# Kernel tuning notes

Measured on AMD Instinct MI355X. Metric: run time of the kernel, lower is better.

## Reference

```python
import jax, jax.numpy as jnp
import numpy as np

N, IN_DIM, H, K = 4096, 64, 64, 3
DT = 0.05


def graph_filter(z, S_powers, W):
    # z: [N, d_in], S_powers: [K, N, N], W: [K, d_in, d_out]
    zk = jnp.einsum('knm,md->knd', S_powers, z)   # K-hop diffused features
    return jnp.einsum('knd,kde->ne', zk, W)       # sum over taps k


def setup_inputs() -> dict:
    key = jax.random.key(0)
    ks = jax.random.split(key, 8)
    w_scale = 0.1
    return {
        'x': jax.random.normal(ks[0], (N, H), jnp.float32),
        'u': jax.random.normal(ks[1], (N, IN_DIM), jnp.float32),
        'S_powers': jax.random.normal(ks[2], (K, N, N), jnp.float32) / np.float32(np.sqrt(N)),
        'WA_hat': jax.random.normal(ks[3], (K, H, H), jnp.float32) * w_scale,
        'WB_hat': jax.random.normal(ks[4], (K, IN_DIM, H), jnp.float32) * w_scale,
        'WA_state': jax.random.normal(ks[5], (K, H, H), jnp.float32) * w_scale,
        'WB_state': jax.random.normal(ks[6], (K, IN_DIM, H), jnp.float32) * w_scale,
        'bx': jnp.zeros((1, H), jnp.float32),
        'bu': jnp.zeros((1, H), jnp.float32),
        'b': jnp.ones((1, H), jnp.float32) * 0.1,
        'n_steps': 4,
    }


def reference(x, u, S_powers, WA_hat, WB_hat, WA_state, WB_state, bx, bu, b, n_steps):
    # Input-driven terms are constant across solver steps; hoist them.
    fu = jax.nn.relu(graph_filter(u, S_powers, WB_hat) + bu)   # [N, H]
    sigma_c = jnp.tanh(graph_filter(u, S_powers, WB_state))    # [N, H]

    def step(xc, _):
        f = jax.nn.relu(graph_filter(xc, S_powers, WA_hat) + bx) + fu
        dx = -(b + f) * xc - graph_filter(xc, S_powers, WA_state) + f * sigma_c
        xn = jnp.clip(xc + DT * dx, -1.0, 1.0)
        return xn, None

    xf, _ = jax.lax.scan(step, x, None, length=n_steps)
    return xf
```

## Files before the change

kernel.cpp:

```cpp
#include <hip/hip_runtime.h>
#include <math.h>


typedef unsigned short u16;
typedef unsigned int u32;
typedef __attribute__((ext_vector_type(8))) short short8;
typedef __attribute__((ext_vector_type(4))) float f32x4;

#define NN 4096
#define HD 64
#define DT_C 0.05f

__device__ __forceinline__ u16 f2bf(float f) {
    u32 u = __float_as_uint(f);
    u += 0x7FFFu + ((u >> 16) & 1u);
    return (u16)(u >> 16);
}
__device__ __forceinline__ u32 pk2(float a, float b) {
    return (u32)f2bf(a) | ((u32)f2bf(b) << 16);
}

__global__ __launch_bounds__(256) void prep_kernel(
    const float* __restrict__ u, const float* __restrict__ x,
    const float* __restrict__ WAh, const float* __restrict__ WAs,
    const float* __restrict__ WBh, const float* __restrict__ WBs,
    u16* __restrict__ ut, u16* __restrict__ xt, u16* __restrict__ Wt)
{
    const int b = blockIdx.x;
    const int t = threadIdx.x;
    if (b < 128) {
        const float* z = (b < 64) ? u : x;
        u16* zt = (b < 64) ? ut : xt;
        const int n0 = (b & 63) * 64;
        __shared__ __align__(16) u16 tile[64][72];
        const int nl = t >> 2, c0 = (t & 3) * 16;
        const float* src = z + (size_t)(n0 + nl) * HD + c0;
        #pragma unroll
        for (int j = 0; j < 16; ++j) tile[nl][c0 + j] = f2bf(src[j]);
        __syncthreads();
        const int h = t >> 2, m0 = (t & 3) * 16;
        uint4 w0, w1;
        w0.x = (u32)tile[m0 + 0][h] | ((u32)tile[m0 + 1][h] << 16);
        w0.y = (u32)tile[m0 + 2][h] | ((u32)tile[m0 + 3][h] << 16);
        w0.z = (u32)tile[m0 + 4][h] | ((u32)tile[m0 + 5][h] << 16);
        w0.w = (u32)tile[m0 + 6][h] | ((u32)tile[m0 + 7][h] << 16);
        w1.x = (u32)tile[m0 + 8][h] | ((u32)tile[m0 + 9][h] << 16);
        w1.y = (u32)tile[m0 + 10][h] | ((u32)tile[m0 + 11][h] << 16);
        w1.z = (u32)tile[m0 + 12][h] | ((u32)tile[m0 + 13][h] << 16);
        w1.w = (u32)tile[m0 + 14][h] | ((u32)tile[m0 + 15][h] << 16);
        u16* dst = zt + (size_t)h * NN + n0 + m0;
        ((uint4*)dst)[0] = w0;
        ((uint4*)dst)[1] = w1;
    } else if (b == 128) {
        for (int f = t; f < 4 * 12288; f += 256) {
            int mat = f / 12288, rem = f % 12288;
            int e = rem / 192, kp = rem % 192;
            const float* Wm = (mat == 0) ? WAh : (mat == 1) ? WAs : (mat == 2) ? WBh : WBs;
            Wt[f] = f2bf(Wm[(size_t)kp * HD + e]);
        }
    }
}

__global__ __launch_bounds__(256) void convS_kernel(
    const float* __restrict__ S, u16* __restrict__ Sb)
{
    const size_t i = ((size_t)blockIdx.x * 256 + threadIdx.x) * 8;
    float4 f0 = *(const float4*)(S + i);
    float4 f1 = *(const float4*)(S + i + 4);
    uint4 o;
    o.x = pk2(f0.x, f0.y); o.y = pk2(f0.z, f0.w);
    o.z = pk2(f1.x, f1.y); o.w = pk2(f1.z, f1.w);
    *(uint4*)(Sb + i) = o;
}

__global__ __launch_bounds__(256) void diffuseA_kernel(
    const u16* __restrict__ Sb, const u16* __restrict__ ut,
    const u16* __restrict__ xt, float* __restrict__ Yp, int kchunk)
{
    const int t = threadIdx.x;
    const int tap = blockIdx.z;
    const int row0 = blockIdx.x * 128;
    const int kb0 = blockIdx.y * kchunk;
    const int w = t >> 6, lane = t & 63, l15 = lane & 15, quad = lane >> 4;

    const u16* A0 = Sb + (size_t)tap * NN * NN + (size_t)(row0 + w * 32 + l15) * NN + quad * 8;
    const u16* A1 = A0 + 16 * NN;

    f32x4 z4 = {0.f, 0.f, 0.f, 0.f};
    f32x4 acc[2][2][4];
    #pragma unroll
    for (int s = 0; s < 2; ++s)
        #pragma unroll
        for (int i = 0; i < 2; ++i)
            #pragma unroll
            for (int j = 0; j < 4; ++j) acc[s][i][j] = z4;

    #pragma unroll 2
    for (int kb = kb0; kb < kb0 + kchunk; kb += 32) {
        short8 a0 = *(const short8*)(A0 + kb);
        short8 a1 = *(const short8*)(A1 + kb);
        #pragma unroll
        for (int ct = 0; ct < 4; ++ct) {
            const size_t bo = (size_t)(ct * 16 + l15) * NN + kb + quad * 8;
            short8 bu = *(const short8*)(ut + bo);
            short8 bx = *(const short8*)(xt + bo);
            acc[0][0][ct] = __builtin_amdgcn_mfma_f32_16x16x32_bf16(a0, bu, acc[0][0][ct], 0, 0, 0);
            acc[0][1][ct] = __builtin_amdgcn_mfma_f32_16x16x32_bf16(a1, bu, acc[0][1][ct], 0, 0, 0);
            acc[1][0][ct] = __builtin_amdgcn_mfma_f32_16x16x32_bf16(a0, bx, acc[1][0][ct], 0, 0, 0);
            acc[1][1][ct] = __builtin_amdgcn_mfma_f32_16x16x32_bf16(a1, bx, acc[1][1][ct], 0, 0, 0);
        }
    }
    #pragma unroll
    for (int s = 0; s < 2; ++s) {
        float* yb = Yp + ((size_t)((blockIdx.y * 3 + tap) * 2 + s) * NN + row0) * HD;
        #pragma unroll
        for (int rt = 0; rt < 2; ++rt)
            #pragma unroll
            for (int ct = 0; ct < 4; ++ct)
                #pragma unroll
                for (int r = 0; r < 4; ++r)
                    yb[(size_t)(w * 32 + rt * 16 + quad * 4 + r) * HD + ct * 16 + l15] = acc[s][rt][ct][r];
    }
}

__global__ __launch_bounds__(256) void diffuseS_kernel(
    const u16* __restrict__ Sb, const u16* __restrict__ xt,
    float* __restrict__ Yp, int kchunk)
{
    const int t = threadIdx.x;
    const int tap = blockIdx.z;
    const int row0 = blockIdx.x * 128;
    const int kb0 = blockIdx.y * kchunk;
    const int w = t >> 6, lane = t & 63, l15 = lane & 15, quad = lane >> 4;

    const u16* A0 = Sb + (size_t)tap * NN * NN + (size_t)(row0 + w * 32 + l15) * NN + quad * 8;
    const u16* A1 = A0 + 16 * NN;

    f32x4 z4 = {0.f, 0.f, 0.f, 0.f};
    f32x4 acc[2][4];
    #pragma unroll
    for (int i = 0; i < 2; ++i)
        #pragma unroll
        for (int j = 0; j < 4; ++j) acc[i][j] = z4;

    #pragma unroll 2
    for (int kb = kb0; kb < kb0 + kchunk; kb += 32) {
        short8 a0 = *(const short8*)(A0 + kb);
        short8 a1 = *(const short8*)(A1 + kb);
        #pragma unroll
        for (int ct = 0; ct < 4; ++ct) {
            short8 bb = *(const short8*)(xt + (size_t)(ct * 16 + l15) * NN + kb + quad * 8);
            acc[0][ct] = __builtin_amdgcn_mfma_f32_16x16x32_bf16(a0, bb, acc[0][ct], 0, 0, 0);
            acc[1][ct] = __builtin_amdgcn_mfma_f32_16x16x32_bf16(a1, bb, acc[1][ct], 0, 0, 0);
        }
    }
    float* yb = Yp + ((size_t)(blockIdx.y * 3 + tap) * NN + row0) * HD;
    #pragma unroll
    for (int rt = 0; rt < 2; ++rt)
        #pragma unroll
        for (int ct = 0; ct < 4; ++ct)
            #pragma unroll
            for (int r = 0; r < 4; ++r)
                yb[(size_t)(w * 32 + rt * 16 + quad * 4 + r) * HD + ct * 16 + l15] = acc[rt][ct][r];
}

__global__ __launch_bounds__(256) void reduce_kernel(
    const float* __restrict__ Yp, int KS, int nsrc,
    u16* __restrict__ dst0, u16* __restrict__ dst1)
{
    const int tid = blockIdx.x * 256 + threadIdx.x;
    const int src = tid / 196608;
    const int r = tid - src * 196608;
    const int d4 = r & 15;
    const int n = (r >> 4) & 4095;
    const int tap = r >> 16;
    const float* p = Yp + ((size_t)tap * nsrc + src) * ((size_t)NN * HD)
                        + (size_t)n * HD + d4 * 4;
    const size_t kstride = (size_t)3 * nsrc * NN * HD;
    float4 s = {0.f, 0.f, 0.f, 0.f};
    for (int ks = 0; ks < KS; ++ks) {
        float4 v = *(const float4*)(p + ks * kstride);
        s.x += v.x; s.y += v.y; s.z += v.z; s.w += v.w;
    }
    u16* dst = src ? dst1 : dst0;
    uint2 o; o.x = pk2(s.x, s.y); o.y = pk2(s.z, s.w);
    *(uint2*)(dst + (size_t)n * 192 + tap * 64 + d4 * 4) = o;
}

__global__ __launch_bounds__(256) void update_step_kernel(
    const u16* __restrict__ Yx,
    const u16* __restrict__ WtAh, const u16* __restrict__ WtAs,
    const float* __restrict__ bx, const float* __restrict__ bvec,
    const float* __restrict__ fu, const float* __restrict__ sc,
    const float* __restrict__ xc, float* __restrict__ xn,
    u16* __restrict__ xtout)
{
    const int t = threadIdx.x;
    const int n0 = blockIdx.x * 64;
    const int w = t >> 6, lane = t & 63, l15 = lane & 15, quad = lane >> 4;
    const u16* Arow = Yx + (size_t)(n0 + w * 16 + l15) * 192 + quad * 8;

    f32x4 z4 = {0.f, 0.f, 0.f, 0.f};
    f32x4 aF[4], aG[4];
    #pragma unroll
    for (int ct = 0; ct < 4; ++ct) { aF[ct] = z4; aG[ct] = z4; }
    #pragma unroll
    for (int s = 0; s < 6; ++s) {
        short8 a = *(const short8*)(Arow + s * 32);
        #pragma unroll
        for (int ct = 0; ct < 4; ++ct) {
            const int wo = (ct * 16 + l15) * 192 + s * 32 + quad * 8;
            short8 bF = *(const short8*)(WtAh + wo);
            short8 bG = *(const short8*)(WtAs + wo);
            aF[ct] = __builtin_amdgcn_mfma_f32_16x16x32_bf16(a, bF, aF[ct], 0, 0, 0);
            aG[ct] = __builtin_amdgcn_mfma_f32_16x16x32_bf16(a, bG, aG[ct], 0, 0, 0);
        }
    }
    #pragma unroll
    for (int ct = 0; ct < 4; ++ct) {
        const int e = ct * 16 + l15;
        const float bxv = bx[e], bbv = bvec[e];
        #pragma unroll
        for (int r = 0; r < 4; ++r) {
            const int n = n0 + w * 16 + quad * 4 + r;
            const size_t o = (size_t)n * HD + e;
            float f = fmaxf(aF[ct][r] + bxv, 0.f) + fu[o];
            float g = aG[ct][r];
            float xv = xc[o];
            float dx = -(bbv + f) * xv - g + f * sc[o];
            float xnv = fminf(fmaxf(xv + DT_C * dx, -1.f), 1.f);
            xn[o] = xnv;
            xtout[(size_t)e * NN + n] = f2bf(xnv);
        }
    }
}

__global__ __launch_bounds__(256) void update1_kernel(
    const u16* __restrict__ Yu, const u16* __restrict__ Yx,
    const u16* __restrict__ WtAh, const u16* __restrict__ WtAs,
    const u16* __restrict__ WtBh, const u16* __restrict__ WtBs,
    const float* __restrict__ bx, const float* __restrict__ bu,
    const float* __restrict__ bvec, const float* __restrict__ x0,
    float* __restrict__ fu, float* __restrict__ sc,
    float* __restrict__ x1, u16* __restrict__ xtout)
{
    const int t = threadIdx.x;
    const int n0 = blockIdx.x * 64;
    const int w = t >> 6, lane = t & 63, l15 = lane & 15, quad = lane >> 4;
    const size_t ao = (size_t)(n0 + w * 16 + l15) * 192 + quad * 8;

    f32x4 z4 = {0.f, 0.f, 0.f, 0.f};
    f32x4 aFu[4], aSc[4], aF[4], aG[4];
    #pragma unroll
    for (int ct = 0; ct < 4; ++ct) { aFu[ct] = z4; aSc[ct] = z4; aF[ct] = z4; aG[ct] = z4; }
    #pragma unroll
    for (int s = 0; s < 6; ++s) {
        short8 au = *(const short8*)(Yu + ao + s * 32);
        short8 ax = *(const short8*)(Yx + ao + s * 32);
        #pragma unroll
        for (int ct = 0; ct < 4; ++ct) {
            const int wo = (ct * 16 + l15) * 192 + s * 32 + quad * 8;
            short8 bFu = *(const short8*)(WtBh + wo);
            short8 bSc = *(const short8*)(WtBs + wo);
            short8 bF  = *(const short8*)(WtAh + wo);
            short8 bG  = *(const short8*)(WtAs + wo);
            aFu[ct] = __builtin_amdgcn_mfma_f32_16x16x32_bf16(au, bFu, aFu[ct], 0, 0, 0);
            aSc[ct] = __builtin_amdgcn_mfma_f32_16x16x32_bf16(au, bSc, aSc[ct], 0, 0, 0);
            aF[ct]  = __builtin_amdgcn_mfma_f32_16x16x32_bf16(ax, bF,  aF[ct],  0, 0, 0);
            aG[ct]  = __builtin_amdgcn_mfma_f32_16x16x32_bf16(ax, bG,  aG[ct],  0, 0, 0);
        }
    }
    #pragma unroll
    for (int ct = 0; ct < 4; ++ct) {
        const int e = ct * 16 + l15;
        const float bxv = bx[e], buv = bu[e], bbv = bvec[e];
        #pragma unroll
        for (int r = 0; r < 4; ++r) {
            const int n = n0 + w * 16 + quad * 4 + r;
            const size_t o = (size_t)n * HD + e;
            float fuv = fmaxf(aFu[ct][r] + buv, 0.f);
            float scv = tanhf(aSc[ct][r]);
            float f = fmaxf(aF[ct][r] + bxv, 0.f) + fuv;
            float g = aG[ct][r];
            float xv = x0[o];
            float dx = -(bbv + f) * xv - g + f * scv;
            float xnv = fminf(fmaxf(xv + DT_C * dx, -1.f), 1.f);
            fu[o] = fuv; sc[o] = scv; x1[o] = xnv;
            xtout[(size_t)e * NN + n] = f2bf(xnv);
        }
    }
}

extern "C" void kernel_launch(void* const* d_in, const int* in_sizes, int n_in,
                              void* d_out, int out_size, void* d_ws, size_t ws_size,
                              hipStream_t stream) {
    const float* x   = (const float*)d_in[0];
    const float* u   = (const float*)d_in[1];
    const float* S   = (const float*)d_in[2];
    const float* WAh = (const float*)d_in[3];
    const float* WBh = (const float*)d_in[4];
    const float* WAs = (const float*)d_in[5];
    const float* WBs = (const float*)d_in[6];
    const float* bx  = (const float*)d_in[7];
    const float* bu  = (const float*)d_in[8];
    const float* bvec= (const float*)d_in[9];
    float* out = (float*)d_out;

    const size_t sbf_bytes = (size_t)3 * NN * NN * 2;
    const size_t slice = (size_t)NN * HD * 4;
    const size_t rest = 2 * 524288 + 98304 + 2 * 1572864 + 4 * 1048576;
    int KS_A = 4, KS_S = 8;
    if (ws_size < sbf_bytes + 24 * slice + rest) { KS_A = 2; KS_S = 4; }
    if (ws_size < sbf_bytes + 12 * slice + rest) { KS_A = 1; KS_S = 2; }
    const int nslice = (KS_A * 6 > KS_S * 3) ? KS_A * 6 : KS_S * 3;

    char* p = (char*)d_ws;
    u16* Sb   = (u16*)p;         p += sbf_bytes;
    float* Yp = (float*)p;       p += (size_t)nslice * slice;
    u16* ut   = (u16*)p;         p += 524288;
    u16* xt   = (u16*)p;         p += 524288;
    u16* Wt   = (u16*)p;         p += 98304;
    u16* Yu   = (u16*)p;         p += 1572864;
    u16* Yx   = (u16*)p;         p += 1572864;
    float* fu = (float*)p;       p += 1048576;
    float* sc = (float*)p;       p += 1048576;
    float* xA = (float*)p;       p += 1048576;
    float* xB = (float*)p;       p += 1048576;

    u16* WtAh = Wt;
    u16* WtAs = Wt + 12288;
    u16* WtBh = Wt + 2 * 12288;
    u16* WtBs = Wt + 3 * 12288;

    prep_kernel<<<130, 256, 0, stream>>>(u, x, WAh, WAs, WBh, WBs, ut, xt, Wt);
    convS_kernel<<<(3 * NN * NN) / (8 * 256), 256, 0, stream>>>(S, Sb);

    diffuseA_kernel<<<dim3(32, KS_A, 3), 256, 0, stream>>>(Sb, ut, xt, Yp, NN / KS_A);
    reduce_kernel<<<1536 / (4 / KS_A > 1 ? 1 : 1), 256, 0, stream>>>(Yp, KS_A, 2, Yu, Yx);
    update1_kernel<<<64, 256, 0, stream>>>(Yu, Yx, WtAh, WtAs, WtBh, WtBs,
                                           bx, bu, bvec, x, fu, sc, xA, xt);
    diffuseS_kernel<<<dim3(32, KS_S, 3), 256, 0, stream>>>(Sb, xt, Yp, NN / KS_S);
    reduce_kernel<<<768, 256, 0, stream>>>(Yp, KS_S, 1, Yx, Yx);
    update_step_kernel<<<64, 256, 0, stream>>>(Yx, WtAh, WtAs, bx, bvec,
                                               fu, sc, xA, xB, xt);
    diffuseS_kernel<<<dim3(32, KS_S, 3), 256, 0, stream>>>(Sb, xt, Yp, NN / KS_S);
    reduce_kernel<<<768, 256, 0, stream>>>(Yp, KS_S, 1, Yx, Yx);
    update_step_kernel<<<64, 256, 0, stream>>>(Yx, WtAh, WtAs, bx, bvec,
                                               fu, sc, xB, xA, xt);
    diffuseS_kernel<<<dim3(32, KS_S, 3), 256, 0, stream>>>(Sb, xt, Yp, NN / KS_S);
    reduce_kernel<<<768, 256, 0, stream>>>(Yp, KS_S, 1, Yx, Yx);
    update_step_kernel<<<64, 256, 0, stream>>>(Yx, WtAh, WtAs, bx, bvec,
                                               fu, sc, xA, out, xt);
}
```

Before: 593.3 us.

## Repack S, features and weights into k-blocked 32-wide slabs for contiguous MFMA loads

```diff
diff --git a/kernel.cpp b/kernel.cpp
--- a/kernel.cpp
+++ b/kernel.cpp
@@ -9,6 +9,7 @@
 
 #define NN 4096
 #define HD 64
+#define KB32 128
 #define DT_C 0.05f
 
 __device__ __forceinline__ u16 f2bf(float f) {
@@ -20,71 +21,93 @@
     return (u32)f2bf(a) | ((u32)f2bf(b) << 16);
 }
 
-__global__ __launch_bounds__(256) void prep_kernel(
+__global__ __launch_bounds__(256) void convS_kernel(
+    const float* __restrict__ S, u16* __restrict__ SbT)
+{
+    const int slab = blockIdx.y;
+    const int tap = slab >> 7, kb = slab & 127;
+    const int t = threadIdx.x;
+    const int n = blockIdx.x * 64 + (t >> 2);
+    const int kq = (t & 3) * 8;
+    const float* src = S + ((size_t)tap * NN + n) * NN + kb * 32 + kq;
+    float4 f0 = ((const float4*)src)[0];
+    float4 f1 = ((const float4*)src)[1];
+    uint4 o;
+    o.x = pk2(f0.x, f0.y); o.y = pk2(f0.z, f0.w);
+    o.z = pk2(f1.x, f1.y); o.w = pk2(f1.z, f1.w);
+    *(uint4*)(SbT + ((size_t)slab * NN + n) * 32 + kq) = o;
+}
+
+__global__ __launch_bounds__(256) void zprep_kernel(
     const float* __restrict__ u, const float* __restrict__ x,
     const float* __restrict__ WAh, const float* __restrict__ WAs,
     const float* __restrict__ WBh, const float* __restrict__ WBs,
-    u16* __restrict__ ut, u16* __restrict__ xt, u16* __restrict__ Wt)
+    u16* __restrict__ utT, u16* __restrict__ xtT, u16* __restrict__ WtT)
 {
     const int b = blockIdx.x;
     const int t = threadIdx.x;
-    if (b < 128) {
-        const float* z = (b < 64) ? u : x;
-        u16* zt = (b < 64) ? ut : xt;
-        const int n0 = (b & 63) * 64;
-        __shared__ __align__(16) u16 tile[64][72];
-        const int nl = t >> 2, c0 = (t & 3) * 16;
+    if (b < 256) {
+        const float* z = (b < 128) ? u : x;
+        u16* ztT = (b < 128) ? utT : xtT;
+        const int kb = b & 127, n0 = kb * 32;
+        __shared__ __align__(16) u16 tile[64][40];
+        const int nl = t >> 3, c0 = (t & 7) * 8;
         const float* src = z + (size_t)(n0 + nl) * HD + c0;
-        #pragma unroll
-        for (int j = 0; j < 16; ++j) tile[nl][c0 + j] = f2bf(src[j]);
+        float4 f0 = ((const float4*)src)[0];
+        float4 f1 = ((const float4*)src)[1];
+        tile[c0 + 0][nl] = f2bf(f0.x); tile[c0 + 1][nl] = f2bf(f0.y);
+        tile[c0 + 2][nl] = f2bf(f0.z); tile[c0 + 3][nl] = f2bf(f0.w);
+        tile[c0 + 4][nl] = f2bf(f1.x); tile[c0 + 5][nl] = f2bf(f1.y);
+        tile[c0 + 6][nl] = f2bf(f1.z); tile[c0 + 7][nl] = f2bf(f1.w);
         __syncthreads();
-        const int h = t >> 2, m0 = (t & 3) * 16;
-        uint4 w0, w1;
-        w0.x = (u32)tile[m0 + 0][h] | ((u32)tile[m0 + 1][h] << 16);
-        w0.y = (u32)tile[m0 + 2][h] | ((u32)tile[m0 + 3][h] << 16);
-        w0.z = (u32)tile[m0 + 4][h] | ((u32)tile[m0 + 5][h] << 16);
-        w0.w = (u32)tile[m0 + 6][h] | ((u32)tile[m0 + 7][h] << 16);
-        w1.x = (u32)tile[m0 + 8][h] | ((u32)tile[m0 + 9][h] << 16);
-        w1.y = (u32)tile[m0 + 10][h] | ((u32)tile[m0 + 11][h] << 16);
-        w1.z = (u32)tile[m0 + 12][h] | ((u32)tile[m0 + 13][h] << 16);
-        w1.w = (u32)tile[m0 + 14][h] | ((u32)tile[m0 + 15][h] << 16);
-        u16* dst = zt + (size_t)h * NN + n0 + m0;
-        ((uint4*)dst)[0] = w0;
-        ((uint4*)dst)[1] = w1;
-    } else if (b == 128) {
-        for (int f = t; f < 4 * 12288; f += 256) {
-            int mat = f / 12288, rem = f % 12288;
-            int e = rem / 192, kp = rem % 192;
+        const int e = t >> 2, kw0 = (t & 3) * 8;
+        short8 v = *(const short8*)&tile[e][kw0];
+        *(short8*)(ztT + ((size_t)kb * 64 + e) * 32 + kw0) = v;
+    } else {
+        for (int f = t; f < 4 * 6 * 64 * 32; f += 256) {
+            int mat = f / 12288, r = f % 12288;
+            int s = r / 2048, r2 = r % 2048;
+            int e = r2 >> 5, kw = r2 & 31;
+            int kp = s * 32 + kw, tap = kp >> 6, d = kp & 63;
             const float* Wm = (mat == 0) ? WAh : (mat == 1) ? WAs : (mat == 2) ? WBh : WBs;
-            Wt[f] = f2bf(Wm[(size_t)kp * HD + e]);
-        }
-    }
-}
-
-__global__ __launch_bounds__(256) void convS_kernel(
-    const float* __restrict__ S, u16* __restrict__ Sb)
-{
-    const size_t i = ((size_t)blockIdx.x * 256 + threadIdx.x) * 8;
-    float4 f0 = *(const float4*)(S + i);
-    float4 f1 = *(const float4*)(S + i + 4);
-    uint4 o;
-    o.x = pk2(f0.x, f0.y); o.y = pk2(f0.z, f0.w);
-    o.z = pk2(f1.x, f1.y); o.w = pk2(f1.z, f1.w);
-    *(uint4*)(Sb + i) = o;
+            WtT[f] = f2bf(Wm[((size_t)tap * HD + d) * HD + e]);
+        }
+    }
+}
+
+__global__ __launch_bounds__(256) void pack_kernel(
+    const float* __restrict__ xn, u16* __restrict__ xtT)
+{
+    const int kb = blockIdx.x, n0 = kb * 32;
+    const int t = threadIdx.x;
+    __shared__ __align__(16) u16 tile[64][40];
+    const int nl = t >> 3, c0 = (t & 7) * 8;
+    const float* src = xn + (size_t)(n0 + nl) * HD + c0;
+    float4 f0 = ((const float4*)src)[0];
+    float4 f1 = ((const float4*)src)[1];
+    tile[c0 + 0][nl] = f2bf(f0.x); tile[c0 + 1][nl] = f2bf(f0.y);
+    tile[c0 + 2][nl] = f2bf(f0.z); tile[c0 + 3][nl] = f2bf(f0.w);
+    tile[c0 + 4][nl] = f2bf(f1.x); tile[c0 + 5][nl] = f2bf(f1.y);
+    tile[c0 + 6][nl] = f2bf(f1.z); tile[c0 + 7][nl] = f2bf(f1.w);
+    __syncthreads();
+    const int e = t >> 2, kw0 = (t & 3) * 8;
+    short8 v = *(const short8*)&tile[e][kw0];
+    *(short8*)(xtT + ((size_t)kb * 64 + e) * 32 + kw0) = v;
 }
 
 __global__ __launch_bounds__(256) void diffuseA_kernel(
-    const u16* __restrict__ Sb, const u16* __restrict__ ut,
-    const u16* __restrict__ xt, float* __restrict__ Yp, int kchunk)
+    const u16* __restrict__ SbT, const u16* __restrict__ utT,
+    const u16* __restrict__ xtT, float* __restrict__ Yp, int iters)
 {
     const int t = threadIdx.x;
     const int tap = blockIdx.z;
     const int row0 = blockIdx.x * 128;
-    const int kb0 = blockIdx.y * kchunk;
+    const int kb0 = blockIdx.y * iters;
     const int w = t >> 6, lane = t & 63, l15 = lane & 15, quad = lane >> 4;
 
-    const u16* A0 = Sb + (size_t)tap * NN * NN + (size_t)(row0 + w * 32 + l15) * NN + quad * 8;
-    const u16* A1 = A0 + 16 * NN;
+    const u16* A0 = SbT + (((size_t)(tap * KB32) * NN + row0 + w * 32 + l15) * 32) + quad * 8;
+    const size_t arowstride = (size_t)NN * 32;
+    const u16* Bu = utT + (size_t)(l15)*0;
 
     f32x4 z4 = {0.f, 0.f, 0.f, 0.f};
     f32x4 acc[2][2][4];
@@ -96,20 +119,23 @@
             for (int j = 0; j < 4; ++j) acc[s][i][j] = z4;
 
     #pragma unroll 2
-    for (int kb = kb0; kb < kb0 + kchunk; kb += 32) {
-        short8 a0 = *(const short8*)(A0 + kb);
-        short8 a1 = *(const short8*)(A1 + kb);
+    for (int it = 0; it < iters; ++it) {
+        const int kb = kb0 + it;
+        const u16* ab = A0 + (size_t)kb * arowstride;
+        short8 a0 = *(const short8*)(ab);
+        short8 a1 = *(const short8*)(ab + 16 * 32);
         #pragma unroll
         for (int ct = 0; ct < 4; ++ct) {
-            const size_t bo = (size_t)(ct * 16 + l15) * NN + kb + quad * 8;
-            short8 bu = *(const short8*)(ut + bo);
-            short8 bx = *(const short8*)(xt + bo);
+            const size_t bo = ((size_t)kb * 64 + ct * 16 + l15) * 32 + quad * 8;
+            short8 bu = *(const short8*)(utT + bo);
+            short8 bx = *(const short8*)(xtT + bo);
             acc[0][0][ct] = __builtin_amdgcn_mfma_f32_16x16x32_bf16(a0, bu, acc[0][0][ct], 0, 0, 0);
             acc[0][1][ct] = __builtin_amdgcn_mfma_f32_16x16x32_bf16(a1, bu, acc[0][1][ct], 0, 0, 0);
             acc[1][0][ct] = __builtin_amdgcn_mfma_f32_16x16x32_bf16(a0, bx, acc[1][0][ct], 0, 0, 0);
             acc[1][1][ct] = __builtin_amdgcn_mfma_f32_16x16x32_bf16(a1, bx, acc[1][1][ct], 0, 0, 0);
         }
     }
+    (void)Bu;
     #pragma unroll
     for (int s = 0; s < 2; ++s) {
         float* yb = Yp + ((size_t)((blockIdx.y * 3 + tap) * 2 + s) * NN + row0) * HD;
@@ -124,17 +150,17 @@
 }
 
 __global__ __launch_bounds__(256) void diffuseS_kernel(
-    const u16* __restrict__ Sb, const u16* __restrict__ xt,
-    float* __restrict__ Yp, int kchunk)
+    const u16* __restrict__ SbT, const u16* __restrict__ xtT,
+    float* __restrict__ Yp, int iters)
 {
     const int t = threadIdx.x;
     const int tap = blockIdx.z;
     const int row0 = blockIdx.x * 128;
-    const int kb0 = blockIdx.y * kchunk;
+    const int kb0 = blockIdx.y * iters;
     const int w = t >> 6, lane = t & 63, l15 = lane & 15, quad = lane >> 4;
 
-    const u16* A0 = Sb + (size_t)tap * NN * NN + (size_t)(row0 + w * 32 + l15) * NN + quad * 8;
-    const u16* A1 = A0 + 16 * NN;
+    const u16* A0 = SbT + (((size_t)(tap * KB32) * NN + row0 + w * 32 + l15) * 32) + quad * 8;
+    const size_t arowstride = (size_t)NN * 32;
 
     f32x4 z4 = {0.f, 0.f, 0.f, 0.f};
     f32x4 acc[2][4];
@@ -144,12 +170,14 @@
         for (int j = 0; j < 4; ++j) acc[i][j] = z4;
 
     #pragma unroll 2
-    for (int kb = kb0; kb < kb0 + kchunk; kb += 32) {
-        short8 a0 = *(const short8*)(A0 + kb);
-        short8 a1 = *(const short8*)(A1 + kb);
+    for (int it = 0; it < iters; ++it) {
+        const int kb = kb0 + it;
+        const u16* ab = A0 + (size_t)kb * arowstride;
+        short8 a0 = *(const short8*)(ab);
+        short8 a1 = *(const short8*)(ab + 16 * 32);
         #pragma unroll
         for (int ct = 0; ct < 4; ++ct) {
-            short8 bb = *(const short8*)(xt + (size_t)(ct * 16 + l15) * NN + kb + quad * 8);
+            short8 bb = *(const short8*)(xtT + ((size_t)kb * 64 + ct * 16 + l15) * 32 + quad * 8);
             acc[0][ct] = __builtin_amdgcn_mfma_f32_16x16x32_bf16(a0, bb, acc[0][ct], 0, 0, 0);
             acc[1][ct] = __builtin_amdgcn_mfma_f32_16x16x32_bf16(a1, bb, acc[1][ct], 0, 0, 0);
         }
@@ -168,37 +196,37 @@
     const float* __restrict__ Yp, int KS, int nsrc,
     u16* __restrict__ dst0, u16* __restrict__ dst1)
 {
-    const int tid = blockIdx.x * 256 + threadIdx.x;
-    const int src = tid / 196608;
-    const int r = tid - src * 196608;
-    const int d4 = r & 15;
-    const int n = (r >> 4) & 4095;
-    const int tap = r >> 16;
-    const float* p = Yp + ((size_t)tap * nsrc + src) * ((size_t)NN * HD)
-                        + (size_t)n * HD + d4 * 4;
+    const int tg = blockIdx.x * 256 + threadIdx.x;
+    const int src = tg / 98304;
+    const int r = tg - src * 98304;
+    const int tap = r >> 15;
+    const int r2 = r & 32767;
+    const int n = r2 >> 3;
+    const int dg = (r2 & 7) * 8;
+    const float* p = Yp + (((size_t)tap * nsrc + src) * NN + n) * HD + dg;
     const size_t kstride = (size_t)3 * nsrc * NN * HD;
-    float4 s = {0.f, 0.f, 0.f, 0.f};
+    float4 s0 = {0.f, 0.f, 0.f, 0.f}, s1 = {0.f, 0.f, 0.f, 0.f};
     for (int ks = 0; ks < KS; ++ks) {
-        float4 v = *(const float4*)(p + ks * kstride);
-        s.x += v.x; s.y += v.y; s.z += v.z; s.w += v.w;
+        float4 v0 = ((const float4*)(p + ks * kstride))[0];
+        float4 v1 = ((const float4*)(p + ks * kstride))[1];
+        s0.x += v0.x; s0.y += v0.y; s0.z += v0.z; s0.w += v0.w;
+        s1.x += v1.x; s1.y += v1.y; s1.z += v1.z; s1.w += v1.w;
     }
     u16* dst = src ? dst1 : dst0;
-    uint2 o; o.x = pk2(s.x, s.y); o.y = pk2(s.z, s.w);
-    *(uint2*)(dst + (size_t)n * 192 + tap * 64 + d4 * 4) = o;
-}
-
-__global__ __launch_bounds__(256) void update_step_kernel(
-    const u16* __restrict__ Yx,
-    const u16* __restrict__ WtAh, const u16* __restrict__ WtAs,
+    uint4 o;
+    o.x = pk2(s0.x, s0.y); o.y = pk2(s0.z, s0.w);
+    o.z = pk2(s1.x, s1.y); o.w = pk2(s1.z, s1.w);
+    *(uint4*)(dst + (((size_t)(tap * 2 + (dg >> 5)) * NN + n) * 32) + (dg & 31)) = o;
+}
+
+__global__ __launch_bounds__(64) void update_step_kernel(
+    const u16* __restrict__ YxT, const u16* __restrict__ WtT,
     const float* __restrict__ bx, const float* __restrict__ bvec,
     const float* __restrict__ fu, const float* __restrict__ sc,
-    const float* __restrict__ xc, float* __restrict__ xn,
-    u16* __restrict__ xtout)
-{
-    const int t = threadIdx.x;
-    const int n0 = blockIdx.x * 64;
-    const int w = t >> 6, lane = t & 63, l15 = lane & 15, quad = lane >> 4;
-    const u16* Arow = Yx + (size_t)(n0 + w * 16 + l15) * 192 + quad * 8;
+    const float* __restrict__ xc, float* __restrict__ xn)
+{
+    const int n0 = blockIdx.x * 16;
+    const int lane = threadIdx.x, l15 = lane & 15, quad = lane >> 4;
 
     f32x4 z4 = {0.f, 0.f, 0.f, 0.f};
     f32x4 aF[4], aG[4];
@@ -206,12 +234,12 @@
     for (int ct = 0; ct < 4; ++ct) { aF[ct] = z4; aG[ct] = z4; }
     #pragma unroll
     for (int s = 0; s < 6; ++s) {
-        short8 a = *(const short8*)(Arow + s * 32);
+        short8 a = *(const short8*)(YxT + (((size_t)s * NN + n0 + l15) * 32) + quad * 8);
         #pragma unroll
         for (int ct = 0; ct < 4; ++ct) {
-            const int wo = (ct * 16 + l15) * 192 + s * 32 + quad * 8;
-            short8 bF = *(const short8*)(WtAh + wo);
-            short8 bG = *(const short8*)(WtAs + wo);
+            const size_t wo = (((size_t)(0 * 6 + s) * 64) + ct * 16 + l15) * 32 + quad * 8;
+            short8 bF = *(const short8*)(WtT + wo);
+            short8 bG = *(const short8*)(WtT + wo + 6 * 64 * 32);
             aF[ct] = __builtin_amdgcn_mfma_f32_16x16x32_bf16(a, bF, aF[ct], 0, 0, 0);
             aG[ct] = __builtin_amdgcn_mfma_f32_16x16x32_bf16(a, bG, aG[ct], 0, 0, 0);
         }
@@ -222,32 +250,26 @@
         const float bxv = bx[e], bbv = bvec[e];
         #pragma unroll
         for (int r = 0; r < 4; ++r) {
-            const int n = n0 + w * 16 + quad * 4 + r;
+            const int n = n0 + quad * 4 + r;
             const size_t o = (size_t)n * HD + e;
             float f = fmaxf(aF[ct][r] + bxv, 0.f) + fu[o];
             float g = aG[ct][r];
             float xv = xc[o];
             float dx = -(bbv + f) * xv - g + f * sc[o];
-            float xnv = fminf(fmaxf(xv + DT_C * dx, -1.f), 1.f);
-            xn[o] = xnv;
-            xtout[(size_t)e * NN + n] = f2bf(xnv);
-        }
-    }
-}
-
-__global__ __launch_bounds__(256) void update1_kernel(
-    const u16* __restrict__ Yu, const u16* __restrict__ Yx,
-    const u16* __restrict__ WtAh, const u16* __restrict__ WtAs,
-    const u16* __restrict__ WtBh, const u16* __restrict__ WtBs,
+            xn[o] = fminf(fmaxf(xv + DT_C * dx, -1.f), 1.f);
+        }
+    }
+}
+
+__global__ __launch_bounds__(64) void update1_kernel(
+    const u16* __restrict__ YuT, const u16* __restrict__ YxT,
+    const u16* __restrict__ WtT,
     const float* __restrict__ bx, const float* __restrict__ bu,
     const float* __restrict__ bvec, const float* __restrict__ x0,
-    float* __restrict__ fu, float* __restrict__ sc,
-    float* __restrict__ x1, u16* __restrict__ xtout)
-{
-    const int t = threadIdx.x;
-    const int n0 = blockIdx.x * 64;
-    const int w = t >> 6, lane = t & 63, l15 = lane & 15, quad = lane >> 4;
-    const size_t ao = (size_t)(n0 + w * 16 + l15) * 192 + quad * 8;
+    float* __restrict__ fu, float* __restrict__ sc, float* __restrict__ x1)
+{
+    const int n0 = blockIdx.x * 16;
+    const int lane = threadIdx.x, l15 = lane & 15, quad = lane >> 4;
 
     f32x4 z4 = {0.f, 0.f, 0.f, 0.f};
     f32x4 aFu[4], aSc[4], aF[4], aG[4];
@@ -255,19 +277,20 @@
     for (int ct = 0; ct < 4; ++ct) { aFu[ct] = z4; aSc[ct] = z4; aF[ct] = z4; aG[ct] = z4; }
     #pragma unroll
     for (int s = 0; s < 6; ++s) {
-        short8 au = *(const short8*)(Yu + ao + s * 32);
-        short8 ax = *(const short8*)(Yx + ao + s * 32);
+        const size_t ao = (((size_t)s * NN + n0 + l15) * 32) + quad * 8;
+        short8 au = *(const short8*)(YuT + ao);
+        short8 ax = *(const short8*)(YxT + ao);
         #pragma unroll
         for (int ct = 0; ct < 4; ++ct) {
-            const int wo = (ct * 16 + l15) * 192 + s * 32 + quad * 8;
-            short8 bFu = *(const short8*)(WtBh + wo);
-            short8 bSc = *(const short8*)(WtBs + wo);
-            short8 bF  = *(const short8*)(WtAh + wo);
-            short8 bG  = *(const short8*)(WtAs + wo);
+            const size_t wo = (((size_t)s * 64) + ct * 16 + l15) * 32 + quad * 8;
+            short8 bF  = *(const short8*)(WtT + wo);
+            short8 bG  = *(const short8*)(WtT + wo + 6 * 64 * 32);
+            short8 bFu = *(const short8*)(WtT + wo + 2 * 6 * 64 * 32);
+            short8 bSc = *(const short8*)(WtT + wo + 3 * 6 * 64 * 32);
+            aF[ct]  = __builtin_amdgcn_mfma_f32_16x16x32_bf16(ax, bF,  aF[ct],  0, 0, 0);
+            aG[ct]  = __builtin_amdgcn_mfma_f32_16x16x32_bf16(ax, bG,  aG[ct],  0, 0, 0);
             aFu[ct] = __builtin_amdgcn_mfma_f32_16x16x32_bf16(au, bFu, aFu[ct], 0, 0, 0);
             aSc[ct] = __builtin_amdgcn_mfma_f32_16x16x32_bf16(au, bSc, aSc[ct], 0, 0, 0);
-            aF[ct]  = __builtin_amdgcn_mfma_f32_16x16x32_bf16(ax, bF,  aF[ct],  0, 0, 0);
-            aG[ct]  = __builtin_amdgcn_mfma_f32_16x16x32_bf16(ax, bG,  aG[ct],  0, 0, 0);
         }
     }
     #pragma unroll
@@ -276,7 +299,7 @@
         const float bxv = bx[e], buv = bu[e], bbv = bvec[e];
         #pragma unroll
         for (int r = 0; r < 4; ++r) {
-            const int n = n0 + w * 16 + quad * 4 + r;
+            const int n = n0 + quad * 4 + r;
             const size_t o = (size_t)n * HD + e;
             float fuv = fmaxf(aFu[ct][r] + buv, 0.f);
             float scv = tanhf(aSc[ct][r]);
@@ -284,9 +307,8 @@
             float g = aG[ct][r];
             float xv = x0[o];
             float dx = -(bbv + f) * xv - g + f * scv;
-            float xnv = fminf(fmaxf(xv + DT_C * dx, -1.f), 1.f);
-            fu[o] = fuv; sc[o] = scv; x1[o] = xnv;
-            xtout[(size_t)e * NN + n] = f2bf(xnv);
+            fu[o] = fuv; sc[o] = scv;
+            x1[o] = fminf(fmaxf(xv + DT_C * dx, -1.f), 1.f);
         }
     }
 }
@@ -315,40 +337,36 @@
     const int nslice = (KS_A * 6 > KS_S * 3) ? KS_A * 6 : KS_S * 3;
 
     char* p = (char*)d_ws;
-    u16* Sb   = (u16*)p;         p += sbf_bytes;
+    u16* SbT  = (u16*)p;         p += sbf_bytes;
     float* Yp = (float*)p;       p += (size_t)nslice * slice;
-    u16* ut   = (u16*)p;         p += 524288;
-    u16* xt   = (u16*)p;         p += 524288;
-    u16* Wt   = (u16*)p;         p += 98304;
-    u16* Yu   = (u16*)p;         p += 1572864;
-    u16* Yx   = (u16*)p;         p += 1572864;
+    u16* utT  = (u16*)p;         p += 524288;
+    u16* xtT  = (u16*)p;         p += 524288;
+    u16* WtT  = (u16*)p;         p += 98304;
+    u16* YuT  = (u16*)p;         p += 1572864;
+    u16* YxT  = (u16*)p;         p += 1572864;
     float* fu = (float*)p;       p += 1048576;
     float* sc = (float*)p;       p += 1048576;
     float* xA = (float*)p;       p += 1048576;
     float* xB = (float*)p;       p += 1048576;
 
-    u16* WtAh = Wt;
-    u16* WtAs = Wt + 12288;
-    u16* WtBh = Wt + 2 * 12288;
-    u16* WtBs = Wt + 3 * 12288;
-
-    prep_kernel<<<130, 256, 0, stream>>>(u, x, WAh, WAs, WBh, WBs, ut, xt, Wt);
-    convS_kernel<<<(3 * NN * NN) / (8 * 256), 256, 0, stream>>>(S, Sb);
-
-    diffuseA_kernel<<<dim3(32, KS_A, 3), 256, 0, stream>>>(Sb, ut, xt, Yp, NN / KS_A);
-    reduce_kernel<<<1536 / (4 / KS_A > 1 ? 1 : 1), 256, 0, stream>>>(Yp, KS_A, 2, Yu, Yx);
-    update1_kernel<<<64, 256, 0, stream>>>(Yu, Yx, WtAh, WtAs, WtBh, WtBs,
-                                           bx, bu, bvec, x, fu, sc, xA, xt);
-    diffuseS_kernel<<<dim3(32, KS_S, 3), 256, 0, stream>>>(Sb, xt, Yp, NN / KS_S);
-    reduce_kernel<<<768, 256, 0, stream>>>(Yp, KS_S, 1, Yx, Yx);
-    update_step_kernel<<<64, 256, 0, stream>>>(Yx, WtAh, WtAs, bx, bvec,
-                                               fu, sc, xA, xB, xt);
-    diffuseS_kernel<<<dim3(32, KS_S, 3), 256, 0, stream>>>(Sb, xt, Yp, NN / KS_S);
-    reduce_kernel<<<768, 256, 0, stream>>>(Yp, KS_S, 1, Yx, Yx);
-    update_step_kernel<<<64, 256, 0, stream>>>(Yx, WtAh, WtAs, bx, bvec,
-                                               fu, sc, xB, xA, xt);
-    diffuseS_kernel<<<dim3(32, KS_S, 3), 256, 0, stream>>>(Sb, xt, Yp, NN / KS_S);
-    reduce_kernel<<<768, 256, 0, stream>>>(Yp, KS_S, 1, Yx, Yx);
-    update_step_kernel<<<64, 256, 0, stream>>>(Yx, WtAh, WtAs, bx, bvec,
-                                               fu, sc, xA, out, xt);
-}
+    zprep_kernel<<<257, 256, 0, stream>>>(u, x, WAh, WAs, WBh, WBs, utT, xtT, WtT);
+    convS_kernel<<<dim3(64, 384), 256, 0, stream>>>(S, SbT);
+
+    diffuseA_kernel<<<dim3(32, KS_A, 3), 256, 0, stream>>>(SbT, utT, xtT, Yp, KB32 / KS_A);
+    reduce_kernel<<<768, 256, 0, stream>>>(Yp, KS_A, 2, YuT, YxT);
+    update1_kernel<<<256, 64, 0, stream>>>(YuT, YxT, WtT, bx, bu, bvec, x, fu, sc, xA);
+    pack_kernel<<<128, 256, 0, stream>>>(xA, xtT);
+    diffuseS_kernel<<<dim3(32, KS_S, 3), 256, 0, stream>>>(SbT, xtT, Yp, KB32 / KS_S);
+    reduce_kernel<<<384, 256, 0, stream>>>(Yp, KS_S, 1, YxT, YxT);
+    update_step_kernel<<<256, 64, 0, stream>>>(YxT, WtT, bx, bvec, fu, sc, xA, xB);
+    pack_kernel<<<128, 256, 0, stream>>>(xB, xtT);
+
+    diffuseS_kernel<<<dim3(32, KS_S, 3), 256, 0, stream>>>(SbT, xtT, Yp, KB32 / KS_S);
+    reduce_kernel<<<384, 256, 0, stream>>>(Yp, KS_S, 1, YxT, YxT);
+    update_step_kernel<<<256, 64, 0, stream>>>(YxT, WtT, bx, bvec, fu, sc, xB, xA);
+    pack_kernel<<<128, 256, 0, stream>>>(xA, xtT);
+
+    diffuseS_kernel<<<dim3(32, KS_S, 3), 256, 0, stream>>>(SbT, xtT, Yp, KB32 / KS_S);
+    reduce_kernel<<<384, 256, 0, stream>>>(Yp, KS_S, 1, YxT, YxT);
+    update_step_kernel<<<256, 64, 0, stream>>>(YxT, WtT, bx, bvec, fu, sc, xA, out);
+}
```

Result: faster. 533.4 us (-10.1%).
